# Optimization experiments

Hardware: AMD Instinct MI355X
Metric: run time of the kernel (lower is better)

## Reference

```python
import jax, jax.numpy as jnp
import numpy as np

CLASS_NUM = 8
OUT_SIZE = 160
EPS = 1e-8


def conv1x1(x, w, b):
    # x: [B,Cin,H,W], w: [Cout,Cin], b: [Cout]
    return jnp.einsum('oc,bchw->bohw', w, x) + b[None, :, None, None]


def setup_inputs() -> dict:
    key = jax.random.key(0)
    ks = jax.random.split(key, 8)
    Cin, Cout = 256, 128
    B, H, W = 16, 80, 80
    feature = jax.random.normal(ks[0], (B, Cin, H, W), dtype=jnp.float32)
    fusion_label = jax.random.randint(ks[1], (B, 1, OUT_SIZE, OUT_SIZE), 0, CLASS_NUM, dtype=jnp.int64) if jax.config.jax_enable_x64 else jax.random.randint(ks[1], (B, 1, OUT_SIZE, OUT_SIZE), 0, CLASS_NUM).astype(jnp.int32)
    w1 = jax.random.normal(ks[2], (2 * Cin, Cin), dtype=jnp.float32) * 0.05
    b1 = jnp.zeros((2 * Cin,), dtype=jnp.float32)
    w2 = jax.random.normal(ks[3], (Cin, 2 * Cin), dtype=jnp.float32) * 0.05
    b2 = jnp.zeros((Cin,), dtype=jnp.float32)
    w3 = jax.random.normal(ks[4], (Cout, Cin), dtype=jnp.float32) * 0.05
    b3 = jnp.zeros((Cout,), dtype=jnp.float32)
    return {"feature": feature, "fusion_label": fusion_label,
            "w1": w1, "b1": b1, "w2": w2, "b2": b2, "w3": w3, "b3": b3}


def reference(feature, fusion_label, w1, b1, w2, b2, w3, b3):
    # 1x1 conv stack with ReLUs (conv1 in the torch module)
    f = jax.nn.relu(conv1x1(feature, w1, b1))
    f = jax.nn.relu(conv1x1(f, w2, b2))
    f2 = jax.nn.relu(conv1x1(f, w3, b3))
    B, C = f2.shape[0], f2.shape[1]
    # bilinear resize, half-pixel centers == torch align_corners=False
    f3 = jax.image.resize(f2, (B, C, OUT_SIZE, OUT_SIZE), method='bilinear', antialias=False)
    # per-class masked mean pooling (segment mean over spatial positions)
    lbl = fusion_label[:, 0]  # [B,H,W]
    onehot = jax.nn.one_hot(lbl, CLASS_NUM, dtype=f3.dtype)  # [B,H,W,K]
    counts = onehot.sum((1, 2))  # [B,K]
    pooled = jnp.einsum('bhwk,bchw->bkc', onehot, f3) / (counts + EPS)[..., None]
    presence = (counts > 0).astype(jnp.int32)  # which (image, class) rows the torch code would emit
    return pooled, presence
```

## Files before the change

### kernel.cpp

```cpp
#include <hip/hip_runtime.h>

#define B_SZ   16
#define P_IN   6400
#define H_IN   80
#define OUTHW  160
#define NCLASS 8

typedef __attribute__((ext_vector_type(8))) short  short8v;
typedef __attribute__((ext_vector_type(4))) float  f32x4;
typedef __attribute__((ext_vector_type(4))) unsigned short ushort4v;
typedef __attribute__((ext_vector_type(2))) unsigned short ushort2v;

__device__ __forceinline__ unsigned short f2bf(float x) {
    union { float f; unsigned int u; } v; v.f = x;
    unsigned int r = v.u + 0x7fffu + ((v.u >> 16) & 1u);
    return (unsigned short)(r >> 16);
}
__device__ __forceinline__ float bf2f(unsigned short h) {
    union { unsigned int u; float f; } v; v.u = ((unsigned int)h) << 16;
    return v.f;
}

__device__ __forceinline__ void gload16(const unsigned short* g, unsigned short* lds) {
    __builtin_amdgcn_global_load_lds(
        (const __attribute__((address_space(1))) unsigned int*)g,
        (__attribute__((address_space(3))) unsigned int*)lds, 16, 0, 0);
}

__global__ void wprep3(const float* __restrict__ w1, const float* __restrict__ w2,
                       const float* __restrict__ w3,
                       unsigned short* __restrict__ h1, unsigned short* __restrict__ l1,
                       unsigned short* __restrict__ h2, unsigned short* __restrict__ l2,
                       unsigned short* __restrict__ h3, unsigned short* __restrict__ l3)
{
    int i = blockIdx.x * 256 + threadIdx.x;
    const float* src; unsigned short *h, *l; int off;
    if (i < 131072)      { src = w1; h = h1; l = l1; off = i; }
    else if (i < 262144) { src = w2; h = h2; l = l2; off = i - 131072; }
    else                 { src = w3; h = h3; l = l3; off = i - 262144;
                           if (off >= 32768) return; }
    float v = src[off];
    unsigned short hi = f2bf(v);
    h[off] = hi;
    l[off] = f2bf(v - bf2f(hi));
}

__global__ void fprep(const float* __restrict__ feat, unsigned short* __restrict__ xh) {
    __shared__ float t[32][257];
    const int b = blockIdx.y, p0 = blockIdx.x * 32;
    const int pi = threadIdx.x & 31, cg = threadIdx.x >> 5;
    const float* fb = feat + (size_t)b * 256 * P_IN;
#pragma unroll 4
    for (int cc = 0; cc < 32; ++cc) {
        int c = cc * 8 + cg;
        t[pi][c] = fb[(size_t)c * P_IN + p0 + pi];
    }
    __syncthreads();
    const int rr  = threadIdx.x >> 7;
    const int cc2 = threadIdx.x & 127;
#pragma unroll 4
    for (int r = 0; r < 32; r += 2) {
        const int row = r + rr;
        ushort2v u;
        u.x = f2bf(t[row][cc2 * 2]);
        u.y = f2bf(t[row][cc2 * 2 + 1]);
        *(ushort2v*)&xh[((size_t)b * P_IN + p0 + row) * 256 + cc2 * 2] = u;
    }
}

template<int K, int NM>
__global__ __launch_bounds__(256, 3)
void conv_mfma(const unsigned short* __restrict__ Wh, const unsigned short* __restrict__ Wl,
               const float* __restrict__ bias,
               const unsigned short* __restrict__ X, unsigned short* __restrict__ Y)
{
    constexpr int M  = NM * 128;
    constexpr int NK = K / 32;
    __shared__ unsigned short As_h[2][4096], As_l[2][4096], Bs[2][4096];
    const int tid = threadIdx.x, lane = tid & 63, w = tid >> 6;
    const int wm = w >> 1, wn = w & 1;

    const int nb = gridDim.x;
    const int id = blockIdx.x;
    const int wg = (id & 7) * (nb >> 3) + (id >> 3);
    const int bb  = wg / (50 * NM);
    const int rem = wg - bb * (50 * NM);
    const int n0 = (rem / NM) * 128;
    const int m0 = (rem - (rem / NM) * NM) * 128;

    const size_t abase = (size_t)m0 * K;
    const size_t xbase = ((size_t)bb * P_IN + n0) * K;

    f32x4 acc[4][4];
#pragma unroll
    for (int i = 0; i < 4; ++i)
#pragma unroll
        for (int j = 0; j < 4; ++j) acc[i][j] = (f32x4)0.f;

    int s_row[2], s_k8[2], s_lo[2];
#pragma unroll
    for (int q = 0; q < 2; ++q) {
        const int ch = 2 * w + q;
        s_row[q] = ch * 16 + (lane >> 2);
        s_k8[q]  = ((((lane & 3) - (s_row[q] >> 1)) & 3) << 3);
        s_lo[q]  = ch * 512;
    }
    int off_a[4], off_b[4];
    const int gsel = lane >> 4;
#pragma unroll
    for (int mi = 0; mi < 4; ++mi) {
        const int r = wm * 64 + mi * 16 + (lane & 15);
        off_a[mi] = r * 32 + (((gsel + (r >> 1)) & 3) << 3);
    }
#pragma unroll
    for (int ni = 0; ni < 4; ++ni) {
        const int r = wn * 64 + ni * 16 + (lane & 15);
        off_b[ni] = r * 32 + (((gsel + (r >> 1)) & 3) << 3);
    }

#define STAGE(buf, kt) do {                                                   \
    _Pragma("unroll")                                                         \
    for (int q = 0; q < 2; ++q) {                                             \
        const size_t kof = (size_t)(kt) * 32 + s_k8[q];                       \
        const size_t gW  = abase + (size_t)s_row[q] * K + kof;                \
        const size_t gX  = xbase + (size_t)s_row[q] * K + kof;                \
        gload16(Wh + gW, &As_h[buf][s_lo[q]]);                                \
        gload16(Wl + gW, &As_l[buf][s_lo[q]]);                                \
        gload16(X  + gX, &Bs[buf][s_lo[q]]);                                  \
    }                                                                         \
} while (0)

    int cur = 0;
    STAGE(0, 0);
    __syncthreads();

    for (int t = 0; t < NK; ++t) {
        if (t + 1 < NK) STAGE(cur ^ 1, t + 1);
        short8v ah[4], al[4], bv[4];
#pragma unroll
        for (int mi = 0; mi < 4; ++mi) {
            ah[mi] = *(const short8v*)&As_h[cur][off_a[mi]];
            al[mi] = *(const short8v*)&As_l[cur][off_a[mi]];
        }
#pragma unroll
        for (int ni = 0; ni < 4; ++ni)
            bv[ni] = *(const short8v*)&Bs[cur][off_b[ni]];
#pragma unroll
        for (int mi = 0; mi < 4; ++mi)
#pragma unroll
            for (int ni = 0; ni < 4; ++ni) {
                acc[mi][ni] = __builtin_amdgcn_mfma_f32_16x16x32_bf16(ah[mi], bv[ni], acc[mi][ni], 0, 0, 0);
                acc[mi][ni] = __builtin_amdgcn_mfma_f32_16x16x32_bf16(al[mi], bv[ni], acc[mi][ni], 0, 0, 0);
            }
        __syncthreads();
        cur ^= 1;
    }
#undef STAGE

    const int lhi = lane >> 4;
#pragma unroll
    for (int mi = 0; mi < 4; ++mi) {
        const int m_base = m0 + wm * 64 + mi * 16 + lhi * 4;
        const float4 b4 = *(const float4*)&bias[m_base];
#pragma unroll
        for (int ni = 0; ni < 4; ++ni) {
            const int n = n0 + wn * 64 + ni * 16 + (lane & 15);
            const size_t o = ((size_t)bb * P_IN + n) * M + m_base;
            ushort4v u;
            u.x = f2bf(fmaxf(acc[mi][ni][0] + b4.x, 0.f));
            u.y = f2bf(fmaxf(acc[mi][ni][1] + b4.y, 0.f));
            u.z = f2bf(fmaxf(acc[mi][ni][2] + b4.z, 0.f));
            u.w = f2bf(fmaxf(acc[mi][ni][3] + b4.w, 0.f));
            *(ushort4v*)&Y[o] = u;
        }
    }
}

__global__ __launch_bounds__(256)
void label_scatter(const int* __restrict__ lbl, float* __restrict__ g,
                   float* __restrict__ counts)
{
    __shared__ float sg[NCLASS][8][80];
    __shared__ float hist[NCLASS];
    const int b = blockIdx.x, slab = blockIdx.y;
    const int tid = threadIdx.x;
    const int r0 = slab * 8;
    for (int i = tid; i < NCLASS * 8 * 80; i += 256) ((float*)sg)[i] = 0.f;
    if (tid < NCLASS) hist[tid] = 0.f;
    __syncthreads();

    const int ibase = 2 * r0 - 1;
    for (int idx = tid; idx < 18 * 160; idx += 256) {
        const int ir = idx / 160, j = idx - ir * 160;
        const int i = ibase + ir;
        if (i < 0 || i >= OUTHW) continue;
        const int k = lbl[(size_t)b * (OUTHW * OUTHW) + i * OUTHW + j];
        const int mi = i >> 1, mj = j >> 1;
        int y0, y1, x0, x1; float wy0, wy1, wx0, wx1;
        if (i & 1) { y0 = mi; y1 = (mi < H_IN - 1) ? mi + 1 : H_IN - 1; wy0 = 0.75f; wy1 = 0.25f; }
        else       { y0 = (mi > 0) ? mi - 1 : 0; y1 = mi;               wy0 = 0.25f; wy1 = 0.75f; }
        if (j & 1) { x0 = mj; x1 = (mj < H_IN - 1) ? mj + 1 : H_IN - 1; wx0 = 0.75f; wx1 = 0.25f; }
        else       { x0 = (mj > 0) ? mj - 1 : 0; x1 = mj;               wx0 = 0.25f; wx1 = 0.75f; }
        if (mi >= r0 && mi < r0 + 8) atomicAdd(&hist[k], 1.f);
        const int ry0 = y0 - r0, ry1 = y1 - r0;
        if (ry0 >= 0 && ry0 < 8) {
            atomicAdd(&sg[k][ry0][x0], wy0 * wx0);
            atomicAdd(&sg[k][ry0][x1], wy0 * wx1);
        }
        if (ry1 >= 0 && ry1 < 8) {
            atomicAdd(&sg[k][ry1][x0], wy1 * wx0);
            atomicAdd(&sg[k][ry1][x1], wy1 * wx1);
        }
    }
    __syncthreads();
    for (int i = tid; i < NCLASS * 8 * 80; i += 256) {
        const int k = i / 640, rem2 = i - k * 640;
        g[((size_t)b * NCLASS + k) * P_IN + r0 * 80 + rem2] = ((const float*)sg)[i];
    }
    if (tid < NCLASS) atomicAdd(&counts[b * NCLASS + tid], hist[tid]);
}

__global__ __launch_bounds__(256)
void pool2(const unsigned short* __restrict__ f3, const float* __restrict__ g,
           float* __restrict__ pooled)
{
    __shared__ float sg[NCLASS][800];
    const int b = blockIdx.x, chunk = blockIdx.y;
    const int tid = threadIdx.x;
#pragma unroll
    for (int i = 0; i < 25; ++i) {
        int idx = i * 256 + tid;
        int k = idx / 800, p = idx - k * 800;
        sg[k][p] = g[((size_t)b * NCLASS + k) * P_IN + chunk * 800 + p];
    }
    __syncthreads();

    const int c  = tid & 127;
    const int kg = tid >> 7;
    float acc0 = 0.f, acc1 = 0.f, acc2 = 0.f, acc3 = 0.f;
    const unsigned short* fb = f3 + ((size_t)b * P_IN + chunk * 800) * 128 + c;
    for (int p = 0; p < 800; ++p) {
        const float fv = bf2f(fb[(size_t)p * 128]);
        acc0 = fmaf(fv, sg[kg * 4 + 0][p], acc0);
        acc1 = fmaf(fv, sg[kg * 4 + 1][p], acc1);
        acc2 = fmaf(fv, sg[kg * 4 + 2][p], acc2);
        acc3 = fmaf(fv, sg[kg * 4 + 3][p], acc3);
    }
    atomicAdd(&pooled[((size_t)b * NCLASS + kg * 4 + 0) * 128 + c], acc0);
    atomicAdd(&pooled[((size_t)b * NCLASS + kg * 4 + 1) * 128 + c], acc1);
    atomicAdd(&pooled[((size_t)b * NCLASS + kg * 4 + 2) * 128 + c], acc2);
    atomicAdd(&pooled[((size_t)b * NCLASS + kg * 4 + 3) * 128 + c], acc3);
}

__global__ void finalize(const float* __restrict__ pooled, const float* __restrict__ counts,
                         float* __restrict__ out)
{
    const int b = blockIdx.x;
#pragma unroll
    for (int i = threadIdx.x; i < NCLASS * 128; i += 256) {
        const int k = i >> 7;
        const float cnt = counts[b * NCLASS + k];
        out[(size_t)b * NCLASS * 128 + i] = pooled[(size_t)b * NCLASS * 128 + i] / (cnt + 1e-8f);
    }
    if (threadIdx.x < NCLASS)
        out[B_SZ * NCLASS * 128 + b * NCLASS + threadIdx.x] =
            (counts[b * NCLASS + threadIdx.x] > 0.f) ? 1.f : 0.f;
}

extern "C" void kernel_launch(void* const* d_in, const int* in_sizes, int n_in,
                              void* d_out, int out_size, void* d_ws, size_t ws_size,
                              hipStream_t stream)
{
    const float* feature = (const float*)d_in[0];
    const int*   lbl     = (const int*)d_in[1];
    const float* w1 = (const float*)d_in[2];
    const float* b1 = (const float*)d_in[3];
    const float* w2 = (const float*)d_in[4];
    const float* b2 = (const float*)d_in[5];
    const float* w3 = (const float*)d_in[6];
    const float* b3 = (const float*)d_in[7];
    float* out = (float*)d_out;

    char* ws = (char*)d_ws;
    unsigned short* Xh  = (unsigned short*)(ws);
    unsigned short* f1  = (unsigned short*)(ws + 52428800);
    unsigned short* f2  = (unsigned short*)(ws + 157286400);
    unsigned short* f3  = (unsigned short*)(ws + 209715200);
    unsigned short* Wh1 = (unsigned short*)(ws + 235929600);
    unsigned short* Wl1 = (unsigned short*)(ws + 236191744);
    unsigned short* Wh2 = (unsigned short*)(ws + 236453888);
    unsigned short* Wl2 = (unsigned short*)(ws + 236716032);
    unsigned short* Wh3 = (unsigned short*)(ws + 236978176);
    unsigned short* Wl3 = (unsigned short*)(ws + 237043712);
    float* g      = (float*)(ws + 237109248);
    float* counts = (float*)(ws + 240386048);
    float* pooled = (float*)(ws + 240386560);

    hipMemsetAsync(counts, 0, 512 + 65536, stream);

    wprep3<<<1152, 256, 0, stream>>>(w1, w2, w3, Wh1, Wl1, Wh2, Wl2, Wh3, Wl3);
    fprep<<<dim3(200, 16), 256, 0, stream>>>(feature, Xh);

    conv_mfma<256, 4><<<3200, 256, 0, stream>>>(Wh1, Wl1, b1, Xh, f1);
    conv_mfma<512, 2><<<1600, 256, 0, stream>>>(Wh2, Wl2, b2, f1, f2);
    conv_mfma<256, 1><<<800,  256, 0, stream>>>(Wh3, Wl3, b3, f2, f3);

    label_scatter<<<dim3(B_SZ, 10), 256, 0, stream>>>(lbl, g, counts);
    pool2<<<dim3(B_SZ, 8), 256, 0, stream>>>(f3, g, pooled);
    finalize<<<B_SZ, 256, 0, stream>>>(pooled, counts, out);
}
```

Before: 396.6 us.

## Fuse feature transpose/bf16 conversion into first conv and use finer waitcnt barriers

Removes the separate fprep kernel that transposed the fp32 feature map to bf16 channel-last. The first conv now loads fp32 feature tiles directly into LDS with a swizzle and converts to bf16 while building MFMA fragments. It also replaces __syncthreads with explicit vmcnt/lgkmcnt waits plus s_barrier in both conv kernels, so the prefetch of the next stage can stay in flight. The cost is twice the LDS for the B tile, lower occupancy (launch bounds 2), and per-element conversion work inside the inner loop.

```diff
diff --git a/kernel.cpp b/kernel.cpp
--- a/kernel.cpp
+++ b/kernel.cpp
@@ -9,7 +9,6 @@
 typedef __attribute__((ext_vector_type(8))) short  short8v;
 typedef __attribute__((ext_vector_type(4))) float  f32x4;
 typedef __attribute__((ext_vector_type(4))) unsigned short ushort4v;
-typedef __attribute__((ext_vector_type(2))) unsigned short ushort2v;
 
 __device__ __forceinline__ unsigned short f2bf(float x) {
     union { float f; unsigned int u; } v; v.f = x;
@@ -21,7 +20,7 @@
     return v.f;
 }
 
-__device__ __forceinline__ void gload16(const unsigned short* g, unsigned short* lds) {
+__device__ __forceinline__ void gload16(const void* g, void* lds) {
     __builtin_amdgcn_global_load_lds(
         (const __attribute__((address_space(1))) unsigned int*)g,
         (__attribute__((address_space(3))) unsigned int*)lds, 16, 0, 0);
@@ -45,26 +44,135 @@
     l[off] = f2bf(v - bf2f(hi));
 }
 
-__global__ void fprep(const float* __restrict__ feat, unsigned short* __restrict__ xh) {
-    __shared__ float t[32][257];
-    const int b = blockIdx.y, p0 = blockIdx.x * 32;
-    const int pi = threadIdx.x & 31, cg = threadIdx.x >> 5;
-    const float* fb = feat + (size_t)b * 256 * P_IN;
-#pragma unroll 4
-    for (int cc = 0; cc < 32; ++cc) {
-        int c = cc * 8 + cg;
-        t[pi][c] = fb[(size_t)c * P_IN + p0 + pi];
-    }
+__global__ __launch_bounds__(256, 2)
+void conv1_fused(const unsigned short* __restrict__ Wh, const unsigned short* __restrict__ Wl,
+                 const float* __restrict__ bias,
+                 const float* __restrict__ F,
+                 unsigned short* __restrict__ Y)
+{
+    constexpr int K = 256, NK = 8, NM = 4, M = 512;
+    __shared__ unsigned short As_h[2][4096], As_l[2][4096];
+    __shared__ float Bf[2][4096];
+    const int tid = threadIdx.x, lane = tid & 63, w = tid >> 6;
+    const int wm = w >> 1, wn = w & 1;
+
+    const int nb = gridDim.x, id = blockIdx.x;
+    const int wg = (id & 7) * (nb >> 3) + (id >> 3);
+    const int bb  = wg / (50 * NM);
+    const int rem = wg - bb * (50 * NM);
+    const int n0 = (rem / NM) * 128;
+    const int m0 = (rem - (rem / NM) * NM) * NM == 0 ? (rem % NM) * 128 : (rem % NM) * 128;
+
+    const size_t abase = (size_t)m0 * K;
+    const size_t fbase = (size_t)bb * 256 * P_IN + n0;
+
+    f32x4 acc[4][4];
+#pragma unroll
+    for (int i = 0; i < 4; ++i)
+#pragma unroll
+        for (int j = 0; j < 4; ++j) acc[i][j] = (f32x4)0.f;
+
+    int a_row[2], a_k8[2], a_lo[2];
+#pragma unroll
+    for (int q = 0; q < 2; ++q) {
+        const int ch = 2 * w + q;
+        a_row[q] = ch * 16 + (lane >> 2);
+        a_k8[q]  = ((((lane & 3) - (a_row[q] >> 1)) & 3) << 3);
+        a_lo[q]  = ch * 512;
+    }
+    int b_k[4], b_src[4], b_lo[4];
+#pragma unroll
+    for (int q = 0; q < 4; ++q) {
+        b_k[q]   = q * 8 + w * 2 + (lane >> 5);
+        const int inrow = (lane & 31) * 4;
+        b_src[q] = inrow ^ ((((b_k[q] >> 3) & 1)) << 4);
+        b_lo[q]  = q * 1024 + w * 256 + lane * 4;
+    }
+    const int gsel = lane >> 4;
+    int off_a[4], bidx[4];
+#pragma unroll
+    for (int mi = 0; mi < 4; ++mi) {
+        const int r = wm * 64 + mi * 16 + (lane & 15);
+        off_a[mi] = r * 32 + (((gsel + (r >> 1)) & 3) << 3);
+    }
+#pragma unroll
+    for (int ni = 0; ni < 4; ++ni) {
+        const int nl = wn * 64 + ni * 16 + (lane & 15);
+        bidx[ni] = ((gsel * 8) * 128 + nl) ^ ((gsel & 1) << 4);
+    }
+
+#define STAGE1(buf, kt) do {                                                  \
+    _Pragma("unroll")                                                         \
+    for (int q = 0; q < 4; ++q) {                                             \
+        const size_t gx = fbase + (size_t)((kt) * 32 + b_k[q]) * P_IN + b_src[q]; \
+        gload16(F + gx, &Bf[buf][b_lo[q]]);                                   \
+    }                                                                         \
+    _Pragma("unroll")                                                         \
+    for (int q = 0; q < 2; ++q) {                                             \
+        const size_t gW = abase + (size_t)a_row[q] * K + (kt) * 32 + a_k8[q]; \
+        gload16(Wh + gW, &As_h[buf][a_lo[q]]);                                \
+        gload16(Wl + gW, &As_l[buf][a_lo[q]]);                                \
+    }                                                                         \
+} while (0)
+
+    int cur = 0;
+    STAGE1(0, 0);
     __syncthreads();
-    const int rr  = threadIdx.x >> 7;
-    const int cc2 = threadIdx.x & 127;
-#pragma unroll 4
-    for (int r = 0; r < 32; r += 2) {
-        const int row = r + rr;
-        ushort2v u;
-        u.x = f2bf(t[row][cc2 * 2]);
-        u.y = f2bf(t[row][cc2 * 2 + 1]);
-        *(ushort2v*)&xh[((size_t)b * P_IN + p0 + row) * 256 + cc2 * 2] = u;
+
+    for (int t = 0; t < NK; ++t) {
+        if (t + 1 < NK) {
+            STAGE1(cur ^ 1, t + 1);
+            asm volatile("s_waitcnt vmcnt(8)" ::: "memory");
+        } else {
+            asm volatile("s_waitcnt vmcnt(0)" ::: "memory");
+        }
+        __builtin_amdgcn_s_barrier();
+        __builtin_amdgcn_sched_barrier(0);
+
+        short8v ah[4], al[4], bv[4];
+#pragma unroll
+        for (int mi = 0; mi < 4; ++mi) {
+            ah[mi] = *(const short8v*)&As_h[cur][off_a[mi]];
+            al[mi] = *(const short8v*)&As_l[cur][off_a[mi]];
+        }
+#pragma unroll
+        for (int ni = 0; ni < 4; ++ni) {
+            union { short8v v; unsigned short u[8]; } pk;
+#pragma unroll
+            for (int j = 0; j < 8; ++j)
+                pk.u[j] = f2bf(Bf[cur][bidx[ni] + j * 128]);
+            bv[ni] = pk.v;
+        }
+#pragma unroll
+        for (int mi = 0; mi < 4; ++mi)
+#pragma unroll
+            for (int ni = 0; ni < 4; ++ni) {
+                acc[mi][ni] = __builtin_amdgcn_mfma_f32_16x16x32_bf16(ah[mi], bv[ni], acc[mi][ni], 0, 0, 0);
+                acc[mi][ni] = __builtin_amdgcn_mfma_f32_16x16x32_bf16(al[mi], bv[ni], acc[mi][ni], 0, 0, 0);
+            }
+        asm volatile("s_waitcnt lgkmcnt(0)" ::: "memory");
+        __builtin_amdgcn_sched_barrier(0);
+        __builtin_amdgcn_s_barrier();
+        cur ^= 1;
+    }
+#undef STAGE1
+
+    const int lhi = lane >> 4;
+#pragma unroll
+    for (int mi = 0; mi < 4; ++mi) {
+        const int m_base = m0 + wm * 64 + mi * 16 + lhi * 4;
+        const float4 b4 = *(const float4*)&bias[m_base];
+#pragma unroll
+        for (int ni = 0; ni < 4; ++ni) {
+            const int n = n0 + wn * 64 + ni * 16 + (lane & 15);
+            const size_t o = ((size_t)bb * P_IN + n) * M + m_base;
+            ushort4v u;
+            u.x = f2bf(fmaxf(acc[mi][ni][0] + b4.x, 0.f));
+            u.y = f2bf(fmaxf(acc[mi][ni][1] + b4.y, 0.f));
+            u.z = f2bf(fmaxf(acc[mi][ni][2] + b4.z, 0.f));
+            u.w = f2bf(fmaxf(acc[mi][ni][3] + b4.w, 0.f));
+            *(ushort4v*)&Y[o] = u;
+        }
     }
 }
 
@@ -80,13 +188,12 @@
     const int tid = threadIdx.x, lane = tid & 63, w = tid >> 6;
     const int wm = w >> 1, wn = w & 1;
 
-    const int nb = gridDim.x;
-    const int id = blockIdx.x;
+    const int nb = gridDim.x, id = blockIdx.x;
     const int wg = (id & 7) * (nb >> 3) + (id >> 3);
     const int bb  = wg / (50 * NM);
     const int rem = wg - bb * (50 * NM);
     const int n0 = (rem / NM) * 128;
-    const int m0 = (rem - (rem / NM) * NM) * 128;
+    const int m0 = (rem % NM) * 128;
 
     const size_t abase = (size_t)m0 * K;
     const size_t xbase = ((size_t)bb * P_IN + n0) * K;
@@ -135,7 +242,15 @@
     __syncthreads();
 
     for (int t = 0; t < NK; ++t) {
-        if (t + 1 < NK) STAGE(cur ^ 1, t + 1);
+        if (t + 1 < NK) {
+            STAGE(cur ^ 1, t + 1);
+            asm volatile("s_waitcnt vmcnt(6)" ::: "memory");
+        } else {
+            asm volatile("s_waitcnt vmcnt(0)" ::: "memory");
+        }
+        __builtin_amdgcn_s_barrier();
+        __builtin_amdgcn_sched_barrier(0);
+
         short8v ah[4], al[4], bv[4];
 #pragma unroll
         for (int mi = 0; mi < 4; ++mi) {
@@ -152,7 +267,9 @@
                 acc[mi][ni] = __builtin_amdgcn_mfma_f32_16x16x32_bf16(ah[mi], bv[ni], acc[mi][ni], 0, 0, 0);
                 acc[mi][ni] = __builtin_amdgcn_mfma_f32_16x16x32_bf16(al[mi], bv[ni], acc[mi][ni], 0, 0, 0);
             }
-        __syncthreads();
+        asm volatile("s_waitcnt lgkmcnt(0)" ::: "memory");
+        __builtin_amdgcn_sched_barrier(0);
+        __builtin_amdgcn_s_barrier();
         cur ^= 1;
     }
 #undef STAGE
@@ -282,26 +399,24 @@
     float* out = (float*)d_out;
 
     char* ws = (char*)d_ws;
-    unsigned short* Xh  = (unsigned short*)(ws);
-    unsigned short* f1  = (unsigned short*)(ws + 52428800);
-    unsigned short* f2  = (unsigned short*)(ws + 157286400);
-    unsigned short* f3  = (unsigned short*)(ws + 209715200);
-    unsigned short* Wh1 = (unsigned short*)(ws + 235929600);
-    unsigned short* Wl1 = (unsigned short*)(ws + 236191744);
-    unsigned short* Wh2 = (unsigned short*)(ws + 236453888);
-    unsigned short* Wl2 = (unsigned short*)(ws + 236716032);
-    unsigned short* Wh3 = (unsigned short*)(ws + 236978176);
-    unsigned short* Wl3 = (unsigned short*)(ws + 237043712);
-    float* g      = (float*)(ws + 237109248);
-    float* counts = (float*)(ws + 240386048);
-    float* pooled = (float*)(ws + 240386560);
+    unsigned short* f1  = (unsigned short*)(ws);
+    unsigned short* f2  = (unsigned short*)(ws + 104857600);
+    unsigned short* f3  = (unsigned short*)(ws + 157286400);
+    unsigned short* Wh1 = (unsigned short*)(ws + 183500800);
+    unsigned short* Wl1 = (unsigned short*)(ws + 183762944);
+    unsigned short* Wh2 = (unsigned short*)(ws + 184025088);
+    unsigned short* Wl2 = (unsigned short*)(ws + 184287232);
+    unsigned short* Wh3 = (unsigned short*)(ws + 184549376);
+    unsigned short* Wl3 = (unsigned short*)(ws + 184614912);
+    float* g      = (float*)(ws + 184680448);
+    float* counts = (float*)(ws + 187957248);
+    float* pooled = (float*)(ws + 187957760);
 
     hipMemsetAsync(counts, 0, 512 + 65536, stream);
 
     wprep3<<<1152, 256, 0, stream>>>(w1, w2, w3, Wh1, Wl1, Wh2, Wl2, Wh3, Wl3);
-    fprep<<<dim3(200, 16), 256, 0, stream>>>(feature, Xh);
-
-    conv_mfma<256, 4><<<3200, 256, 0, stream>>>(Wh1, Wl1, b1, Xh, f1);
+
+    conv1_fused<<<3200, 256, 0, stream>>>(Wh1, Wl1, b1, feature, f1);
     conv_mfma<512, 2><<<1600, 256, 0, stream>>>(Wh2, Wl2, b2, f1, f2);
     conv_mfma<256, 1><<<800,  256, 0, stream>>>(Wh3, Wl3, b3, f2, f3);
 
```

New measurement: 404.4 us. Within noise of the previous version (+2.0%).
